# Kernel tuning notes

Hardware: AMD Instinct MI355X
Metric: run time of the kernel (lower is better)

## Reference

```python
import jax, jax.numpy as jnp
import numpy as np

B, C, N = 8, 2048, 512

def setup_inputs() -> dict:
    key = jax.random.key(0)
    ks = jax.random.split(key, 7)
    s = 1.0 / np.sqrt(N)
    return {
        "x":  jax.random.normal(ks[0], (B, C, N), dtype=jnp.float32),
        "Wq": jax.random.normal(ks[1], (N, N), dtype=jnp.float32) * s,
        "bq": jax.random.normal(ks[2], (N,), dtype=jnp.float32) * 0.01,
        "Wk": jax.random.normal(ks[3], (N, N), dtype=jnp.float32) * s,
        "bk": jax.random.normal(ks[4], (N,), dtype=jnp.float32) * 0.01,
        "Wv": jax.random.normal(ks[5], (N, N), dtype=jnp.float32) * s,
        "bv": jax.random.normal(ks[6], (N,), dtype=jnp.float32) * 0.01,
    }

def reference(x, Wq, bq, Wk, bk, Wv, bv):
    b, c, n = x.shape
    # QKV projections (torch Linear: x @ W.T + b)
    q = jnp.einsum('bcn,mn->bcm', x, Wq) + bq
    k = jnp.einsum('bcn,mn->bcm', x, Wk) + bk
    v = jnp.einsum('bcn,mn->bcm', x, Wv) + bv
    # attention over the C (token) dim: [b, c, c]
    attn = jnp.einsum('bcn,bdn->bcd', q, k)
    attn = jax.nn.softmax(attn, axis=-1) / jnp.sqrt(jnp.float32(n))
    # dropout is identity in eval mode
    out = jnp.einsum('bcd,bdn->bcn', attn, v)  # [b, c, n]
    # faithful to torch: .transpose(1, 2).reshape(B, C, N)
    score = jnp.transpose(out, (0, 2, 1)).reshape(b, c, n)
    return score
```

## Files before the change

kernel.cpp:

```cpp
#include <hip/hip_runtime.h>


typedef _Float16 half_t;
typedef __attribute__((ext_vector_type(8))) _Float16 half8;
typedef __attribute__((ext_vector_type(4))) _Float16 half4;
typedef __attribute__((ext_vector_type(4))) float    f32x4;

#define MFMA16x32(A_, B_, C_) __builtin_amdgcn_mfma_f32_16x16x32_f16((A_), (B_), (C_), 0, 0, 0)

__device__ __forceinline__ void gload_lds16(const void* g, void* l) {
  __builtin_amdgcn_global_load_lds(
      (const __attribute__((address_space(1))) void*)g,
      (__attribute__((address_space(3))) void*)l, 16, 0, 0);
}

__global__ void cast_f16(const float* __restrict__ src, half_t* __restrict__ dst,
                         int total4) {
  int idx = blockIdx.x * 256 + threadIdx.x;
  if (idx >= total4) return;
  f32x4 v = ((const f32x4*)src)[idx];
  half4 h;
#pragma unroll
  for (int j = 0; j < 4; ++j) h[j] = (_Float16)v[j];
  *(half4*)&dst[(size_t)idx * 4] = h;
}

template <int NKT, int SA, int SB, int MR>
__device__ __forceinline__ void gemm_core(
    const char* Abytes, const char* Bbytes,
    half_t* At, half_t* Bt, int tid, f32x4 (&acc)[MR][4]) {
  const int lane = tid & 63;
  const int wv = tid >> 6;
  const int g = lane >> 4, li = lane & 15;
  const int wm = wv >> 1, wn = wv & 1;
  const int ASTRIDE = MR * 2048;

  auto STAGE = [&](int kc, int buf) {
#pragma unroll
    for (int i2 = 0; i2 < MR; ++i2) {
      int seg = i2 * 256 + tid;
      int row = seg >> 3, blk = seg & 7;
      int bsrc = blk ^ (row & 7);
      gload_lds16(Abytes + ((size_t)row * SA + kc + bsrc * 8) * 2,
                  (void*)&At[buf * ASTRIDE + seg * 8]);
    }
#pragma unroll
    for (int i2 = 0; i2 < 4; ++i2) {
      int seg = i2 * 256 + tid;
      int row = seg >> 3, blk = seg & 7;
      int bsrc = blk ^ (row & 7);
      gload_lds16(Bbytes + ((size_t)row * SB + kc + bsrc * 8) * 2,
                  (void*)&Bt[buf * 8192 + seg * 8]);
    }
  };

  STAGE(0, 0);
  __syncthreads();
  int cur = 0;
#pragma unroll 1
  for (int kt = 0; kt < NKT; ++kt) {
    if (kt + 1 < NKT) STAGE((kt + 1) * 64, cur ^ 1);
#pragma unroll
    for (int kk = 0; kk < 2; ++kk) {
      half8 af[MR], bf[4];
#pragma unroll
      for (int i = 0; i < MR; ++i) {
        int ar = wm * (MR * 16) + i * 16 + li;
        af[i] = *(const half8*)&At[cur * ASTRIDE + ar * 64 + (((4 * kk + g) ^ (ar & 7)) * 8)];
      }
#pragma unroll
      for (int j = 0; j < 4; ++j) {
        int br = wn * 64 + j * 16 + li;
        bf[j] = *(const half8*)&Bt[cur * 8192 + br * 64 + (((4 * kk + g) ^ (br & 7)) * 8)];
      }
#pragma unroll
      for (int i = 0; i < MR; ++i)
#pragma unroll
        for (int j = 0; j < 4; ++j) acc[i][j] = MFMA16x32(af[i], bf[j], acc[i][j]);
    }
    __syncthreads();
    cur ^= 1;
  }
}

template <int MODE>
__global__ __launch_bounds__(256) void proj_gemm(
    const half_t* __restrict__ A, const half_t* __restrict__ Bm,
    const float* __restrict__ bias, half_t* __restrict__ out) {
  __shared__ half_t At[2 * 4 * 2048];
  __shared__ half_t Bt[2 * 8192];
  const int tid = threadIdx.x;
  const int lane = tid & 63, wv = tid >> 6;
  const int g = lane >> 4, li = lane & 15;
  const int wm = wv >> 1, wn = wv & 1;
  const int M0 = blockIdx.x * 128, N0 = blockIdx.y * 128;

  const f32x4 kZero = {0.f, 0.f, 0.f, 0.f};
  f32x4 acc[4][4];
#pragma unroll
  for (int i = 0; i < 4; ++i)
#pragma unroll
    for (int j = 0; j < 4; ++j) acc[i][j] = kZero;

  gemm_core<8, 512, 512, 4>((const char*)(A + (size_t)M0 * 512),
                            (const char*)(Bm + (size_t)N0 * 512), At, Bt, tid, acc);

  if (MODE == 2) {
#pragma unroll
    for (int i = 0; i < 4; ++i) {
      int trow = M0 + wm * 64 + i * 16 + 4 * g;
#pragma unroll
      for (int j = 0; j < 4; ++j) {
        int m = N0 + wn * 64 + j * 16 + li;
        float bs = bias[m];
#pragma unroll
        for (int r = 0; r < 4; ++r) {
          out[(size_t)(trow + r) * 512 + m] = (_Float16)(acc[i][j][r] + bs);
        }
      }
    }
  } else {
#pragma unroll
    for (int i = 0; i < 4; ++i) {
      int m0r = M0 + wm * 64 + i * 16 + 4 * g;
#pragma unroll
      for (int r = 0; r < 4; ++r) {
        int m = m0r + r;
        float bs = bias[m];
#pragma unroll
        for (int j = 0; j < 4; ++j) {
          int t = N0 + wn * 64 + j * 16 + li;
          out[(size_t)m * 16384 + t] = (_Float16)(acc[i][j][r] + bs);
        }
      }
    }
  }
}

__global__ __launch_bounds__(256) void s_gemm(
    const half_t* __restrict__ q, const half_t* __restrict__ k,
    float* __restrict__ S, int co) {
  __shared__ half_t At[2 * 2 * 2048];
  __shared__ half_t Bt[2 * 8192];
  const int tid = threadIdx.x;
  const int lane = tid & 63, wv = tid >> 6;
  const int g = lane >> 4, li = lane & 15;
  const int wm = wv >> 1, wn = wv & 1;
  const int id = blockIdx.x;
  const int b = id & 7;
  const int idx = id >> 3;
  const int M0 = (idx & 15) * 64;
  const int N0 = (idx >> 4) * 128;

  const f32x4 kZero = {0.f, 0.f, 0.f, 0.f};
  f32x4 acc[2][4];
#pragma unroll
  for (int i = 0; i < 2; ++i)
#pragma unroll
    for (int j = 0; j < 4; ++j) acc[i][j] = kZero;

  gemm_core<8, 512, 512, 2>(
      (const char*)(q + (size_t)(b * 2048 + co + M0) * 512),
      (const char*)(k + (size_t)(b * 2048 + N0) * 512), At, Bt, tid, acc);

  float* Sb = S + (size_t)(b * 1024 + M0) * 2048 + N0;
#pragma unroll
  for (int i = 0; i < 2; ++i) {
#pragma unroll
    for (int j = 0; j < 4; ++j) {
#pragma unroll
      for (int r = 0; r < 4; ++r) {
        Sb[(size_t)(wm * 32 + i * 16 + 4 * g + r) * 2048 + wn * 64 + j * 16 + li] =
            acc[i][j][r];
      }
    }
  }
}

__global__ __launch_bounds__(256) void softmax_rows(
    float* __restrict__ S, float* __restrict__ lbuf) {
  const int rr = blockIdx.x * 4 + (threadIdx.x >> 6);
  const int lane = threadIdx.x & 63;
  float* Srow = S + (size_t)rr * 2048;

  f32x4 v[8];
#pragma unroll
  for (int it = 0; it < 8; ++it) v[it] = *(const f32x4*)&Srow[lane * 4 + it * 256];

  float mx = -3e38f;
#pragma unroll
  for (int it = 0; it < 8; ++it)
    mx = fmaxf(mx, fmaxf(fmaxf(v[it][0], v[it][1]), fmaxf(v[it][2], v[it][3])));
  mx = fmaxf(mx, __shfl_xor(mx, 1));
  mx = fmaxf(mx, __shfl_xor(mx, 2));
  mx = fmaxf(mx, __shfl_xor(mx, 4));
  mx = fmaxf(mx, __shfl_xor(mx, 8));
  mx = fmaxf(mx, __shfl_xor(mx, 16));
  mx = fmaxf(mx, __shfl_xor(mx, 32));

  float sum = 0.f;
  half4 h[8];
#pragma unroll
  for (int it = 0; it < 8; ++it) {
#pragma unroll
    for (int j = 0; j < 4; ++j) {
      float p = __expf(v[it][j] - mx);
      sum += p;
      h[it][j] = (_Float16)p;
    }
  }
  sum += __shfl_xor(sum, 1);
  sum += __shfl_xor(sum, 2);
  sum += __shfl_xor(sum, 4);
  sum += __shfl_xor(sum, 8);
  sum += __shfl_xor(sum, 16);
  sum += __shfl_xor(sum, 32);

  half_t* P = (half_t*)S;
#pragma unroll
  for (int it = 0; it < 8; ++it)
    *(half4*)&P[(size_t)rr * 4096 + lane * 4 + it * 256] = h[it];
  if (lane == 0) lbuf[rr] = sum;
}

__global__ __launch_bounds__(256) void pv_gemm(
    const half_t* __restrict__ P, const half_t* __restrict__ vt,
    const float* __restrict__ lbuf, float* __restrict__ outp, int co) {
  __shared__ half_t At[2 * 2 * 2048];
  __shared__ half_t Bt[2 * 8192];
  const int tid = threadIdx.x;
  const int lane = tid & 63, wv = tid >> 6;
  const int g = lane >> 4, li = lane & 15;
  const int wm = wv >> 1, wn = wv & 1;
  const int id = blockIdx.x;
  const int b = id & 7;
  const int idx = id >> 3;
  const int M0 = (idx >> 2) * 64;
  const int N0 = (idx & 3) * 128;

  const f32x4 kZero = {0.f, 0.f, 0.f, 0.f};
  f32x4 acc[2][4];
#pragma unroll
  for (int i = 0; i < 2; ++i)
#pragma unroll
    for (int j = 0; j < 4; ++j) acc[i][j] = kZero;

  gemm_core<32, 4096, 16384, 2>(
      (const char*)(P + (size_t)(b * 1024 + M0) * 4096),
      (const char*)(vt + (size_t)N0 * 16384 + (size_t)b * 2048), At, Bt, tid, acc);

#pragma unroll
  for (int i = 0; i < 2; ++i) {
    int c0r = M0 + wm * 32 + i * 16 + 4 * g;
    float inv[4];
#pragma unroll
    for (int r = 0; r < 4; ++r)
      inv[r] = 1.0f / (lbuf[b * 1024 + c0r + r] * 22.62741699796952f);
#pragma unroll
    for (int j = 0; j < 4; ++j) {
      int n = N0 + wn * 64 + j * 16 + li;
      float* ob = outp + (size_t)b * 1048576 + (size_t)n * 2048 + co + c0r;
#pragma unroll
      for (int r = 0; r < 4; ++r) {
        ob[r] = acc[i][j][r] * inv[r];
      }
    }
  }
}

extern "C" void kernel_launch(void* const* d_in, const int* in_sizes, int n_in,
                              void* d_out, int out_size, void* d_ws, size_t ws_size,
                              hipStream_t stream) {
  const float* x  = (const float*)d_in[0];
  const float* Wq = (const float*)d_in[1];
  const float* bq = (const float*)d_in[2];
  const float* Wk = (const float*)d_in[3];
  const float* bk = (const float*)d_in[4];
  const float* Wv = (const float*)d_in[5];
  const float* bv = (const float*)d_in[6];

  half_t* qsb  = (half_t*)d_ws;
  half_t* ksb  = qsb + (size_t)16384 * 512;
  half_t* vtb  = ksb + (size_t)16384 * 512;
  half_t* xh   = vtb + (size_t)512 * 16384;
  half_t* wqh  = xh  + (size_t)16384 * 512;
  half_t* wkh  = wqh + (size_t)512 * 512;
  half_t* wvh  = wkh + (size_t)512 * 512;
  float*  Sbuf = (float*)xh;
  float*  lbuf = (float*)(((char*)d_ws) + (size_t)117 * 1024 * 1024);

  cast_f16<<<dim3(16384 * 512 / 4 / 256), 256, 0, stream>>>(x, xh, 16384 * 512 / 4);
  cast_f16<<<dim3(512 * 512 / 4 / 256), 256, 0, stream>>>(Wq, wqh, 512 * 512 / 4);
  cast_f16<<<dim3(512 * 512 / 4 / 256), 256, 0, stream>>>(Wk, wkh, 512 * 512 / 4);
  cast_f16<<<dim3(512 * 512 / 4 / 256), 256, 0, stream>>>(Wv, wvh, 512 * 512 / 4);

  proj_gemm<2><<<dim3(128, 4), 256, 0, stream>>>(xh, wqh, bq, qsb);
  proj_gemm<2><<<dim3(128, 4), 256, 0, stream>>>(xh, wkh, bk, ksb);
  proj_gemm<1><<<dim3(4, 128), 256, 0, stream>>>(wvh, xh, bv, vtb);

  for (int chunk = 0; chunk < 2; ++chunk) {
    const int co = chunk * 1024;
    s_gemm<<<dim3(2048), 256, 0, stream>>>(qsb, ksb, Sbuf, co);
    softmax_rows<<<dim3(2048), 256, 0, stream>>>(Sbuf, lbuf);
    pv_gemm<<<dim3(512), 256, 0, stream>>>((const half_t*)Sbuf, vtb, lbuf,
                                           (float*)d_out, co);
  }
}
```

Baseline: 206.0 us.

## Fuse QK^T with online softmax and rescale P tiles inside PV GEMM

Replaces the separate S GEMM, which wrote fp32 scores, and the softmax pass with one kernel. It computes QK^T tiles with a resident Q block in LDS and keeps online max/sum per 64-column tile, writing fp16 probabilities plus per-tile maxima. A small merge kernel combines the two column halves, and the PV GEMM rescales each P tile by exp(m_tile - m_global) while staging it into LDS. The two chunk passes and the four cast launches are also collapsed into single launches. This removes the fp32 score round trip and several launches, but adds per-tile scaling work in PV and runs the fused kernel with only 512 blocks and a 64KB+ LDS footprint, which may limit occupancy.

```diff
diff --git a/kernel.cpp b/kernel.cpp
--- a/kernel.cpp
+++ b/kernel.cpp
@@ -14,15 +14,53 @@
       (__attribute__((address_space(3))) void*)l, 16, 0, 0);
 }
 
-__global__ void cast_f16(const float* __restrict__ src, half_t* __restrict__ dst,
-                         int total4) {
+__device__ __forceinline__ float dpp_max16(float x) {
+  int t;
+  t = __builtin_amdgcn_update_dpp(__float_as_int(x), __float_as_int(x), 0xB1, 0xF, 0xF, false);
+  x = fmaxf(x, __int_as_float(t));
+  t = __builtin_amdgcn_update_dpp(__float_as_int(x), __float_as_int(x), 0x4E, 0xF, 0xF, false);
+  x = fmaxf(x, __int_as_float(t));
+  t = __builtin_amdgcn_update_dpp(__float_as_int(x), __float_as_int(x), 0x124, 0xF, 0xF, false);
+  x = fmaxf(x, __int_as_float(t));
+  t = __builtin_amdgcn_update_dpp(__float_as_int(x), __float_as_int(x), 0x128, 0xF, 0xF, false);
+  x = fmaxf(x, __int_as_float(t));
+  return x;
+}
+
+__device__ __forceinline__ float dpp_sum16(float x) {
+  int t;
+  t = __builtin_amdgcn_update_dpp(__float_as_int(x), __float_as_int(x), 0xB1, 0xF, 0xF, false);
+  x += __int_as_float(t);
+  t = __builtin_amdgcn_update_dpp(__float_as_int(x), __float_as_int(x), 0x4E, 0xF, 0xF, false);
+  x += __int_as_float(t);
+  t = __builtin_amdgcn_update_dpp(__float_as_int(x), __float_as_int(x), 0x124, 0xF, 0xF, false);
+  x += __int_as_float(t);
+  t = __builtin_amdgcn_update_dpp(__float_as_int(x), __float_as_int(x), 0x128, 0xF, 0xF, false);
+  x += __int_as_float(t);
+  return x;
+}
+
+__global__ void cast_all(const float* __restrict__ x, const float* __restrict__ Wq,
+                         const float* __restrict__ Wk, const float* __restrict__ Wv,
+                         half_t* __restrict__ xh, half_t* __restrict__ wqh,
+                         half_t* __restrict__ wkh, half_t* __restrict__ wvh) {
   int idx = blockIdx.x * 256 + threadIdx.x;
-  if (idx >= total4) return;
-  f32x4 v = ((const f32x4*)src)[idx];
+  const float* s;
+  half_t* d;
+  int off;
+  if (idx < 2097152) { s = x; d = xh; off = idx; }
+  else {
+    int w = idx - 2097152;
+    int which = w >> 16;
+    off = w & 65535;
+    s = (which == 0) ? Wq : (which == 1) ? Wk : Wv;
+    d = (which == 0) ? wqh : (which == 1) ? wkh : wvh;
+  }
+  f32x4 v = ((const f32x4*)s)[off];
   half4 h;
 #pragma unroll
   for (int j = 0; j < 4; ++j) h[j] = (_Float16)v[j];
-  *(half4*)&dst[(size_t)idx * 4] = h;
+  *(half4*)&d[(size_t)off * 4] = h;
 }
 
 template <int NKT, int SA, int SB, int MR>
@@ -137,97 +175,138 @@
   }
 }
 
-__global__ __launch_bounds__(256) void s_gemm(
+__global__ __launch_bounds__(256) void s_softmax(
     const half_t* __restrict__ q, const half_t* __restrict__ k,
-    float* __restrict__ S, int co) {
-  __shared__ half_t At[2 * 2 * 2048];
-  __shared__ half_t Bt[2 * 8192];
+    half_t* __restrict__ Pp, float* __restrict__ m_t,
+    float* __restrict__ m_fin, float* __restrict__ l_h) {
+  __shared__ half_t At[64 * 512];
+  __shared__ half_t Bt[2][64 * 64];
   const int tid = threadIdx.x;
   const int lane = tid & 63, wv = tid >> 6;
   const int g = lane >> 4, li = lane & 15;
-  const int wm = wv >> 1, wn = wv & 1;
   const int id = blockIdx.x;
   const int b = id & 7;
-  const int idx = id >> 3;
-  const int M0 = (idx & 15) * 64;
-  const int N0 = (idx >> 4) * 128;
-
+  const int rest = id >> 3;
+  const int M0 = (rest >> 1) * 64;
+  const int h = rest & 1;
+  const int d0 = h * 1024;
+
+  const char* qb = (const char*)(q + (size_t)(b * 2048 + M0) * 512);
+  const char* kb = (const char*)(k + (size_t)(b * 2048 + d0) * 512);
+
+#pragma unroll
+  for (int i2 = 0; i2 < 16; ++i2) {
+    int seg = i2 * 256 + tid;
+    int row = seg >> 6, blk = seg & 63;
+    int bsrc = blk ^ (row & 7);
+    gload_lds16(qb + ((size_t)row * 512 + bsrc * 8) * 2, (void*)&At[seg * 8]);
+  }
+
+  auto BSTAGE = [&](int it, int buf) {
+    int dt = it >> 3, ks = it & 7;
+#pragma unroll
+    for (int i2 = 0; i2 < 2; ++i2) {
+      int seg = i2 * 256 + tid;
+      int row = seg >> 3, blk = seg & 7;
+      int bsrc = blk ^ (row & 7);
+      gload_lds16(kb + ((size_t)(dt * 64 + row) * 512 + ks * 64 + bsrc * 8) * 2,
+                  (void*)&Bt[buf][seg * 8]);
+    }
+  };
+  BSTAGE(0, 0);
+  __syncthreads();
+
+  const int ar = wv * 16 + li;
+  const int swzA = ar & 7;
   const f32x4 kZero = {0.f, 0.f, 0.f, 0.f};
-  f32x4 acc[2][4];
-#pragma unroll
-  for (int i = 0; i < 2; ++i)
-#pragma unroll
-    for (int j = 0; j < 4; ++j) acc[i][j] = kZero;
-
-  gemm_core<8, 512, 512, 2>(
-      (const char*)(q + (size_t)(b * 2048 + co + M0) * 512),
-      (const char*)(k + (size_t)(b * 2048 + N0) * 512), At, Bt, tid, acc);
-
-  float* Sb = S + (size_t)(b * 1024 + M0) * 2048 + N0;
-#pragma unroll
-  for (int i = 0; i < 2; ++i) {
-#pragma unroll
-    for (int j = 0; j < 4; ++j) {
+  float m_run[4] = {-3e38f, -3e38f, -3e38f, -3e38f};
+  float l_run[4] = {0.f, 0.f, 0.f, 0.f};
+  f32x4 acc[4];
+  int cur = 0;
+
+#pragma unroll 1
+  for (int it = 0; it < 128; ++it) {
+    const int dt = it >> 3, ks = it & 7;
+    if (ks == 0) {
+#pragma unroll
+      for (int j = 0; j < 4; ++j) acc[j] = kZero;
+    }
+    if (it + 1 < 128) BSTAGE(it + 1, cur ^ 1);
+
+#pragma unroll
+    for (int kk = 0; kk < 2; ++kk) {
+      half8 af = *(const half8*)&At[ar * 512 + (((ks * 8 + kk * 4 + g) ^ swzA) * 8)];
+#pragma unroll
+      for (int j = 0; j < 4; ++j) {
+        int br = j * 16 + li;
+        half8 bf = *(const half8*)&Bt[cur][br * 64 + (((kk * 4 + g) ^ (br & 7)) * 8)];
+        acc[j] = MFMA16x32(af, bf, acc[j]);
+      }
+    }
+
+    if (ks == 7) {
+      float mnew[4], alpha[4], tsum[4];
 #pragma unroll
       for (int r = 0; r < 4; ++r) {
-        Sb[(size_t)(wm * 32 + i * 16 + 4 * g + r) * 2048 + wn * 64 + j * 16 + li] =
-            acc[i][j][r];
-      }
-    }
-  }
-}
-
-__global__ __launch_bounds__(256) void softmax_rows(
-    float* __restrict__ S, float* __restrict__ lbuf) {
-  const int rr = blockIdx.x * 4 + (threadIdx.x >> 6);
-  const int lane = threadIdx.x & 63;
-  float* Srow = S + (size_t)rr * 2048;
-
-  f32x4 v[8];
-#pragma unroll
-  for (int it = 0; it < 8; ++it) v[it] = *(const f32x4*)&Srow[lane * 4 + it * 256];
-
-  float mx = -3e38f;
-#pragma unroll
-  for (int it = 0; it < 8; ++it)
-    mx = fmaxf(mx, fmaxf(fmaxf(v[it][0], v[it][1]), fmaxf(v[it][2], v[it][3])));
-  mx = fmaxf(mx, __shfl_xor(mx, 1));
-  mx = fmaxf(mx, __shfl_xor(mx, 2));
-  mx = fmaxf(mx, __shfl_xor(mx, 4));
-  mx = fmaxf(mx, __shfl_xor(mx, 8));
-  mx = fmaxf(mx, __shfl_xor(mx, 16));
-  mx = fmaxf(mx, __shfl_xor(mx, 32));
-
-  float sum = 0.f;
-  half4 h[8];
-#pragma unroll
-  for (int it = 0; it < 8; ++it) {
-#pragma unroll
-    for (int j = 0; j < 4; ++j) {
-      float p = __expf(v[it][j] - mx);
-      sum += p;
-      h[it][j] = (_Float16)p;
-    }
-  }
-  sum += __shfl_xor(sum, 1);
-  sum += __shfl_xor(sum, 2);
-  sum += __shfl_xor(sum, 4);
-  sum += __shfl_xor(sum, 8);
-  sum += __shfl_xor(sum, 16);
-  sum += __shfl_xor(sum, 32);
-
-  half_t* P = (half_t*)S;
-#pragma unroll
-  for (int it = 0; it < 8; ++it)
-    *(half4*)&P[(size_t)rr * 4096 + lane * 4 + it * 256] = h[it];
-  if (lane == 0) lbuf[rr] = sum;
+        float tm = fmaxf(fmaxf(acc[0][r], acc[1][r]), fmaxf(acc[2][r], acc[3][r]));
+        tm = dpp_max16(tm);
+        mnew[r] = fmaxf(m_run[r], tm);
+        alpha[r] = __expf(m_run[r] - mnew[r]);
+        tsum[r] = 0.f;
+      }
+      const size_t prow0 = (size_t)(b * 2048 + M0 + wv * 16);
+#pragma unroll
+      for (int j = 0; j < 4; ++j) {
+#pragma unroll
+        for (int r = 0; r < 4; ++r) {
+          float p = __expf(acc[j][r] - mnew[r]);
+          tsum[r] += p;
+          Pp[(prow0 + 4 * g + r) * 2048 + d0 + dt * 64 + j * 16 + li] = (_Float16)p;
+        }
+      }
+#pragma unroll
+      for (int r = 0; r < 4; ++r) {
+        float ts = dpp_sum16(tsum[r]);
+        l_run[r] = l_run[r] * alpha[r] + ts;
+        m_run[r] = mnew[r];
+      }
+      if (li == 0) {
+#pragma unroll
+        for (int r = 0; r < 4; ++r)
+          m_t[(prow0 + 4 * g + r) * 32 + h * 16 + dt] = mnew[r];
+      }
+    }
+
+    __syncthreads();
+    cur ^= 1;
+  }
+
+  if (li == 0) {
+    const size_t prow0 = (size_t)(b * 2048 + M0 + wv * 16);
+#pragma unroll
+    for (int r = 0; r < 4; ++r) {
+      m_fin[(prow0 + 4 * g + r) * 2 + h] = m_run[r];
+      l_h[(prow0 + 4 * g + r) * 2 + h] = l_run[r];
+    }
+  }
+}
+
+__global__ void sm_merge(const float* __restrict__ m_fin, const float* __restrict__ l_h,
+                         float* __restrict__ m_glob, float* __restrict__ l_fin) {
+  int rr = blockIdx.x * 256 + threadIdx.x;
+  float m0 = m_fin[rr * 2], m1 = m_fin[rr * 2 + 1];
+  float mg = fmaxf(m0, m1);
+  l_fin[rr] = l_h[rr * 2] * __expf(m0 - mg) + l_h[rr * 2 + 1] * __expf(m1 - mg);
+  m_glob[rr] = mg;
 }
 
 __global__ __launch_bounds__(256) void pv_gemm(
-    const half_t* __restrict__ P, const half_t* __restrict__ vt,
-    const float* __restrict__ lbuf, float* __restrict__ outp, int co) {
-  __shared__ half_t At[2 * 2 * 2048];
-  __shared__ half_t Bt[2 * 8192];
+    const half_t* __restrict__ Pp, const half_t* __restrict__ vt,
+    const float* __restrict__ m_t, const float* __restrict__ m_glob,
+    const float* __restrict__ l_fin, float* __restrict__ outp) {
+  __shared__ half_t At[2][2 * 2048];
+  __shared__ half_t Bt[2][8192];
+  __shared__ float  sc[64][33];
   const int tid = threadIdx.x;
   const int lane = tid & 63, wv = tid >> 6;
   const int g = lane >> 4, li = lane & 15;
@@ -237,6 +316,44 @@
   const int idx = id >> 3;
   const int M0 = (idx >> 2) * 64;
   const int N0 = (idx & 3) * 128;
+  const int rgb = b * 2048 + M0;
+
+#pragma unroll
+  for (int i2 = 0; i2 < 8; ++i2) {
+    int e = i2 * 256 + tid;
+    int row = e >> 5, kt = e & 31;
+    sc[row][kt] = __expf(m_t[(size_t)(rgb + row) * 32 + kt] - m_glob[rgb + row]);
+  }
+
+  const half_t* Pb = Pp + (size_t)rgb * 2048;
+  const char* Bb = (const char*)(vt + (size_t)N0 * 16384 + (size_t)b * 2048);
+
+  auto BSTAGE = [&](int kt, int buf) {
+#pragma unroll
+    for (int i2 = 0; i2 < 4; ++i2) {
+      int seg = i2 * 256 + tid;
+      int row = seg >> 3, blk = seg & 7;
+      int bsrc = blk ^ (row & 7);
+      gload_lds16(Bb + ((size_t)row * 16384 + kt * 64 + bsrc * 8) * 2,
+                  (void*)&Bt[buf][seg * 8]);
+    }
+  };
+  const int s0row = tid >> 3, s0blk = tid & 7;
+  const int s1row = (256 + tid) >> 3, s1blk = tid & 7;
+
+  __syncthreads();
+
+  half8 a0 = *(const half8*)&Pb[(size_t)s0row * 2048 + s0blk * 8];
+  half8 a1 = *(const half8*)&Pb[(size_t)s1row * 2048 + s1blk * 8];
+  BSTAGE(0, 0);
+  {
+    _Float16 f0 = (_Float16)sc[s0row][0], f1 = (_Float16)sc[s1row][0];
+#pragma unroll
+    for (int e = 0; e < 8; ++e) { a0[e] *= f0; a1[e] *= f1; }
+    *(half8*)&At[0][s0row * 64 + ((s0blk ^ (s0row & 7)) * 8)] = a0;
+    *(half8*)&At[0][s1row * 64 + ((s1blk ^ (s1row & 7)) * 8)] = a1;
+  }
+  __syncthreads();
 
   const f32x4 kZero = {0.f, 0.f, 0.f, 0.f};
   f32x4 acc[2][4];
@@ -245,9 +362,43 @@
 #pragma unroll
     for (int j = 0; j < 4; ++j) acc[i][j] = kZero;
 
-  gemm_core<32, 4096, 16384, 2>(
-      (const char*)(P + (size_t)(b * 1024 + M0) * 4096),
-      (const char*)(vt + (size_t)N0 * 16384 + (size_t)b * 2048), At, Bt, tid, acc);
+  int cur = 0;
+#pragma unroll 1
+  for (int kt = 0; kt < 32; ++kt) {
+    half8 n0, n1;
+    if (kt + 1 < 32) {
+      n0 = *(const half8*)&Pb[(size_t)s0row * 2048 + (kt + 1) * 64 + s0blk * 8];
+      n1 = *(const half8*)&Pb[(size_t)s1row * 2048 + (kt + 1) * 64 + s1blk * 8];
+      BSTAGE(kt + 1, cur ^ 1);
+    }
+#pragma unroll
+    for (int kk = 0; kk < 2; ++kk) {
+      half8 af[2], bf[4];
+#pragma unroll
+      for (int i = 0; i < 2; ++i) {
+        int arr = wm * 32 + i * 16 + li;
+        af[i] = *(const half8*)&At[cur][arr * 64 + (((4 * kk + g) ^ (arr & 7)) * 8)];
+      }
+#pragma unroll
+      for (int j = 0; j < 4; ++j) {
+        int br = wn * 64 + j * 16 + li;
+        bf[j] = *(const half8*)&Bt[cur][br * 64 + (((4 * kk + g) ^ (br & 7)) * 8)];
+      }
+#pragma unroll
+      for (int i = 0; i < 2; ++i)
+#pragma unroll
+        for (int j = 0; j < 4; ++j) acc[i][j] = MFMA16x32(af[i], bf[j], acc[i][j]);
+    }
+    if (kt + 1 < 32) {
+      _Float16 f0 = (_Float16)sc[s0row][kt + 1], f1 = (_Float16)sc[s1row][kt + 1];
+#pragma unroll
+      for (int e = 0; e < 8; ++e) { n0[e] *= f0; n1[e] *= f1; }
+      *(half8*)&At[cur ^ 1][s0row * 64 + ((s0blk ^ (s0row & 7)) * 8)] = n0;
+      *(half8*)&At[cur ^ 1][s1row * 64 + ((s1blk ^ (s1row & 7)) * 8)] = n1;
+    }
+    __syncthreads();
+    cur ^= 1;
+  }
 
 #pragma unroll
   for (int i = 0; i < 2; ++i) {
@@ -255,11 +406,11 @@
     float inv[4];
 #pragma unroll
     for (int r = 0; r < 4; ++r)
-      inv[r] = 1.0f / (lbuf[b * 1024 + c0r + r] * 22.62741699796952f);
+      inv[r] = 1.0f / (l_fin[b * 2048 + c0r + r] * 22.62741699796952f);
 #pragma unroll
     for (int j = 0; j < 4; ++j) {
       int n = N0 + wn * 64 + j * 16 + li;
-      float* ob = outp + (size_t)b * 1048576 + (size_t)n * 2048 + co + c0r;
+      float* ob = outp + (size_t)b * 1048576 + (size_t)n * 2048 + c0r;
 #pragma unroll
       for (int r = 0; r < 4; ++r) {
         ob[r] = acc[i][j][r] * inv[r];
@@ -282,27 +433,25 @@
   half_t* qsb  = (half_t*)d_ws;
   half_t* ksb  = qsb + (size_t)16384 * 512;
   half_t* vtb  = ksb + (size_t)16384 * 512;
-  half_t* xh   = vtb + (size_t)512 * 16384;
+  half_t* Pp   = vtb + (size_t)512 * 16384;
+  half_t* xh   = Pp;
   half_t* wqh  = xh  + (size_t)16384 * 512;
   half_t* wkh  = wqh + (size_t)512 * 512;
   half_t* wvh  = wkh + (size_t)512 * 512;
-  float*  Sbuf = (float*)xh;
-  float*  lbuf = (float*)(((char*)d_ws) + (size_t)117 * 1024 * 1024);
-
-  cast_f16<<<dim3(16384 * 512 / 4 / 256), 256, 0, stream>>>(x, xh, 16384 * 512 / 4);
-  cast_f16<<<dim3(512 * 512 / 4 / 256), 256, 0, stream>>>(Wq, wqh, 512 * 512 / 4);
-  cast_f16<<<dim3(512 * 512 / 4 / 256), 256, 0, stream>>>(Wk, wkh, 512 * 512 / 4);
-  cast_f16<<<dim3(512 * 512 / 4 / 256), 256, 0, stream>>>(Wv, wvh, 512 * 512 / 4);
+  float*  m_t  = (float*)(Pp + (size_t)16384 * 2048);
+  float*  m_fin = m_t + (size_t)16384 * 32;
+  float*  l_hb  = m_fin + (size_t)16384 * 2;
+  float*  m_glb = l_hb + (size_t)16384 * 2;
+  float*  l_fin = m_glb + (size_t)16384;
+
+  cast_all<<<dim3(8960), 256, 0, stream>>>(x, Wq, Wk, Wv, xh, wqh, wkh, wvh);
 
   proj_gemm<2><<<dim3(128, 4), 256, 0, stream>>>(xh, wqh, bq, qsb);
   proj_gemm<2><<<dim3(128, 4), 256, 0, stream>>>(xh, wkh, bk, ksb);
   proj_gemm<1><<<dim3(4, 128), 256, 0, stream>>>(wvh, xh, bv, vtb);
 
-  for (int chunk = 0; chunk < 2; ++chunk) {
-    const int co = chunk * 1024;
-    s_gemm<<<dim3(2048), 256, 0, stream>>>(qsb, ksb, Sbuf, co);
-    softmax_rows<<<dim3(2048), 256, 0, stream>>>(Sbuf, lbuf);
-    pv_gemm<<<dim3(512), 256, 0, stream>>>((const half_t*)Sbuf, vtb, lbuf,
-                                           (float*)d_out, co);
-  }
-}
+  s_softmax<<<dim3(512), 256, 0, stream>>>(qsb, ksb, Pp, m_t, m_fin, l_hb);
+  sm_merge<<<dim3(64), 256, 0, stream>>>(m_fin, l_hb, m_glb, l_fin);
+  pv_gemm<<<dim3(1024), 256, 0, stream>>>(Pp, vtb, m_t, m_glb, l_fin,
+                                          (float*)d_out);
+}
```

New measurement: 216.6 us. 5.1% more time.
